# Kernel optimization log

Hardware: AMD Instinct MI355X
Metric: run time of the kernel (lower is better)

## Reference

```python
import jax, jax.numpy as jnp
import numpy as np

N = 30000      # nodes
E = 480000     # edges
H = 128        # hidden_nf
NQ = 7         # qubits
D = 2 ** NQ    # 128, quantum state dim == embedding_size
NL = 2         # block n_layers (QGCL layers)
QL = 2         # quantum circuit layers inside each QGCL
NORM = 100.0   # normalization_factor ('sum' aggregation)
NORM_CONST = 1.0


def _cnot_perm_indices(n):
    # Composed permutation for CNOT(0,1)...CNOT(n-2,n-1), CNOT(n-1,0).
    # PennyLane convention: wire 0 is the most significant bit.
    idx = np.arange(2 ** n)
    pairs = [(i, i + 1) for i in range(n - 1)] + [(n - 1, 0)]
    g = None
    for c, t in pairs:
        cb = (idx >> (n - 1 - c)) & 1
        f = idx ^ (cb << (n - 1 - t))  # flip target bit if control set (involution)
        g = f if g is None else g[f]
    return g

_CNOT_G = jnp.asarray(_cnot_perm_indices(NQ))


def _quantum_states(q_in, coeffs, A_re, A_im):
    """Vectorized VQC over all nodes. q_in [N,D] real -> [N,D] complex state."""
    norm = jnp.sqrt(jnp.sum(q_in ** 2, axis=1, keepdims=True) + 1e-12)
    s = (q_in / norm).astype(jnp.complex64)  # normalized initial state per node
    I = jnp.eye(D, dtype=jnp.complex64)
    for j in range(QL):
        # Cayley transform -> unitary
        A = (A_re[j] + 1j * A_im[j]).astype(jnp.complex64)
        A = A + A.conj().T
        q = (A - 1j * I) @ jnp.linalg.inv(A + 1j * I)
        # single-qubit layer: RY(b) @ RX(a) on every qubit -> kron power
        a, b = coeffs[j, 0].astype(jnp.complex64), coeffs[j, 1].astype(jnp.complex64)
        ca, sa = jnp.cos(a / 2), jnp.sin(a / 2)
        cb, sb = jnp.cos(b / 2), jnp.sin(b / 2)
        RX = jnp.stack([jnp.stack([ca, -1j * sa]), jnp.stack([-1j * sa, ca])])
        RY = jnp.stack([jnp.stack([cb, -sb]), jnp.stack([sb, cb])])
        G = RY @ RX
        Gk = G
        for _ in range(NQ - 1):
            Gk = jnp.kron(Gk, G)
        s = s @ q.T            # QubitUnitary
        s = s @ Gk.T           # RX/RY on all qubits
        s = s[:, _CNOT_G]      # CNOT ring (pure permutation)
    return s


def setup_inputs() -> dict:
    key = jax.random.key(0)
    ks = jax.random.split(key, 20)
    return {
        "h": jax.random.normal(ks[0], (N, H), jnp.float32),
        "x": jax.random.normal(ks[1], (N, 3), jnp.float32),
        "edge_index": jax.random.randint(ks[2], (2, E), 0, N, jnp.int32),
        "edge_attr": jax.random.normal(ks[3], (E, 1), jnp.float32),
        "e_w1": jax.random.normal(ks[4], (NL, 2 * H + 2, H), jnp.float32) * 0.05,
        "e_b1": jnp.zeros((NL, H), jnp.float32),
        "e_w2": jax.random.normal(ks[5], (NL, H, H), jnp.float32) * 0.05,
        "e_b2": jnp.zeros((NL, H), jnp.float32),
        "enc_w": jax.random.normal(ks[6], (NL, 2 * H, D), jnp.float32) * 0.05,
        "enc_b": jnp.zeros((NL, D), jnp.float32),
        "coeffs": jax.random.normal(ks[7], (NL, QL, 2), jnp.float32) * 0.1,
        "A_re": jax.random.normal(ks[8], (NL, QL, D, D), jnp.float32) * 0.01,
        "A_im": jax.random.normal(ks[9], (NL, QL, D, D), jnp.float32) * 0.01,
        "dec_w": jax.random.normal(ks[10], (NL, D, H), jnp.float32) * 0.05,
        "dec_b": jnp.zeros((NL, H), jnp.float32),
        "c_w1": jax.random.normal(ks[11], (2 * H + 2, H), jnp.float32) * 0.05,
        "c_b1": jnp.zeros((H,), jnp.float32),
        "c_w2": jax.random.normal(ks[12], (H, H), jnp.float32) * 0.05,
        "c_b2": jnp.zeros((H,), jnp.float32),
        "c_w3": jax.random.normal(ks[13], (H, 1), jnp.float32) * 0.001,  # xavier gain=0.001
    }


def reference(h, x, edge_index, edge_attr, e_w1, e_b1, e_w2, e_b2, enc_w, enc_b,
              coeffs, A_re, A_im, dec_w, dec_b, c_w1, c_b1, c_w2, c_b2, c_w3):
    row, col = edge_index[0], edge_index[1]
    # coord2diff
    diff = x[row] - x[col]
    radial = jnp.sum(diff ** 2, axis=1, keepdims=True)     # [E,1] (used as 'distances')
    coord_diff = diff / (jnp.sqrt(radial + 1e-8) + NORM_CONST)
    eattr = jnp.concatenate([radial, edge_attr], axis=1)   # [E,2]

    for l in range(NL):  # QGCL layers
        m = jnp.concatenate([h[row], h[col], eattr], axis=1)       # [E, 2H+2]
        m = jax.nn.silu(m @ e_w1[l] + e_b1[l])
        m = jax.nn.silu(m @ e_w2[l] + e_b2[l])                     # edge messages mij
        agg = jax.ops.segment_sum(m, row, num_segments=N) / NORM   # scatter-add
        q_in = jnp.concatenate([h, agg], axis=1) @ enc_w[l] + enc_b[l]
        # quantum part is detached in the original (torch .detach + re-tensor)
        qs = jax.lax.stop_gradient(
            _quantum_states(q_in, coeffs[l], A_re[l], A_im[l]))
        h = h + qs.real.astype(h.dtype) @ dec_w[l] + dec_b[l]

    # EquivariantUpdate (tanh=False)
    t = jnp.concatenate([h[row], h[col], eattr], axis=1)
    t = jax.nn.silu(t @ c_w1 + c_b1)
    t = jax.nn.silu(t @ c_w2 + c_b2)
    t = t @ c_w3                                                   # [E,1]
    trans = coord_diff * t
    x = x + jax.ops.segment_sum(trans, row, num_segments=N) / NORM
    return h, x
```

## Files before the change

kernel.cpp:

```cpp
#include <hip/hip_runtime.h>
#include <math.h>

#define N_NODES 30000
#define N_EDGES 480000
#define HDIM 128
#define EPB 64
#define AS 296
#define NAS 264
#define MS 136

typedef __attribute__((ext_vector_type(8))) short short8b;
typedef __attribute__((ext_vector_type(4))) float f32x4;

__device__ __forceinline__ float silu_f(float v) {
  return v / (1.0f + __expf(-v));
}

__device__ __forceinline__ unsigned short f2bf(float f) {
  unsigned int u = __float_as_uint(f);
  unsigned int r = u + 0x7fffu + ((u >> 16) & 1u);
  return (unsigned short)(r >> 16);
}

__global__ void init_out_bf_kernel(const float* __restrict__ h,
                                   const float* __restrict__ x,
                                   float* __restrict__ out,
                                   ushort* __restrict__ hbf) {
  int idx = blockIdx.x * 256 + threadIdx.x;
  float4 v = ((const float4*)h)[idx];
  ((float4*)out)[idx] = v;
  ushort4 o;
  o.x = f2bf(v.x); o.y = f2bf(v.y); o.z = f2bf(v.z); o.w = f2bf(v.w);
  ((ushort4*)hbf)[idx] = o;
  if (idx < N_NODES * 3 / 4) {
    ((float4*)(out + N_NODES * HDIM))[idx] = ((const float4*)x)[idx];
  }
}

__global__ void convert_all_kernel(
    const float* __restrict__ e_w1, const float* __restrict__ e_w2,
    const float* __restrict__ enc_w, const float* __restrict__ c_w1,
    const float* __restrict__ c_w2,
    ushort* __restrict__ w1cs, ushort* __restrict__ w2cs,
    ushort* __restrict__ enccs, ushort* __restrict__ cw1cs,
    ushort* __restrict__ cw2cs) {
  int idx = blockIdx.x * 256 + threadIdx.x;
  if (idx >= 55 * 4096) return;
  int ci = idx >> 12, rem = idx & 4095, n = rem >> 5, kk = rem & 31;
  const float* W;
  ushort* dst;
  int Kreal, ktl;
  if (ci < 18) {
    int l = ci / 9; ktl = ci - l * 9;
    W = e_w1 + (size_t)l * 258 * HDIM; dst = w1cs + (size_t)l * 9 * 4096;
    Kreal = 258;
  } else if (ci < 26) {
    int c2 = ci - 18; int l = c2 >> 2; ktl = c2 & 3;
    W = e_w2 + (size_t)l * HDIM * HDIM; dst = w2cs + (size_t)l * 4 * 4096;
    Kreal = 128;
  } else if (ci < 42) {
    int c2 = ci - 26; int l = c2 >> 3; ktl = c2 & 7;
    W = enc_w + (size_t)l * 256 * HDIM; dst = enccs + (size_t)l * 8 * 4096;
    Kreal = 256;
  } else if (ci < 51) {
    ktl = ci - 42; W = c_w1; dst = cw1cs; Kreal = 258;
  } else {
    ktl = ci - 51; W = c_w2; dst = cw2cs; Kreal = 128;
  }
  int k = ktl * 32 + kk;
  float v = (k < Kreal) ? W[(size_t)k * HDIM + n] : 0.0f;
  dst[ktl * 4096 + rem] = f2bf(v);
}

__global__ void count_kernel(const int* __restrict__ ei, int* __restrict__ cursor) {
  int e = blockIdx.x * 256 + threadIdx.x;
  atomicAdd(&cursor[ei[e]], 1);
}

__global__ __launch_bounds__(1024) void scan_kernel(int* __restrict__ cursor,
                                                    int* __restrict__ cstart) {
  __shared__ int sums[1024];
  const int tid = threadIdx.x;
  const int base = tid * 30;
  int local[30];
  int s = 0;
#pragma unroll
  for (int j = 0; j < 30; ++j) {
    int idx = base + j;
    int d = (idx < N_NODES) ? cursor[idx] : 0;
    local[j] = s;
    s += d;
  }
  sums[tid] = s;
  __syncthreads();
  for (int off = 1; off < 1024; off <<= 1) {
    int add = (tid >= off) ? sums[tid - off] : 0;
    __syncthreads();
    sums[tid] += add;
    __syncthreads();
  }
  int excl = (tid == 0) ? 0 : sums[tid - 1];
#pragma unroll
  for (int j = 0; j < 30; ++j) {
    int idx = base + j;
    if (idx < N_NODES) {
      int v = excl + local[j];
      cursor[idx] = v;
      cstart[idx] = v;
    }
  }
}

__global__ void fill_kernel(const int* __restrict__ ei, int* __restrict__ cursor,
                            int* __restrict__ elist) {
  int e = blockIdx.x * 256 + threadIdx.x;
  int r = ei[e];
  int pos = atomicAdd(&cursor[r], 1);
  elist[pos] = e;
}

__global__ void ns_init_kernel(const float* __restrict__ Are,
                               const float* __restrict__ Aim,
                               float2* __restrict__ X) {
  int lj = blockIdx.y;
  int idx = blockIdx.x * 256 + threadIdx.x;
  int r = idx >> 7, c = idx & 127;
  const float* are = Are + (size_t)lj * 16384;
  const float* aim = Aim + (size_t)lj * 16384;
  float re = are[r * 128 + c] + are[c * 128 + r];
  float im = aim[r * 128 + c] - aim[c * 128 + r];
  if (r == c) im -= 1.0f;
  X[(size_t)lj * 16384 + idx] = make_float2(re, im);
}

__global__ void ns_bx_kernel(const float* __restrict__ Are,
                             const float* __restrict__ Aim,
                             const float2* __restrict__ X,
                             float2* __restrict__ T) {
  int lj = blockIdx.y;
  int idx = blockIdx.x * 256 + threadIdx.x;
  int r = idx >> 7, c = idx & 127;
  const float* are = Are + (size_t)lj * 16384;
  const float* aim = Aim + (size_t)lj * 16384;
  const float2* x = X + (size_t)lj * 16384;
  float2 acc = make_float2(0.f, 0.f);
  for (int k = 0; k < 128; ++k) {
    float re = are[r * 128 + k] + are[k * 128 + r];
    float im = aim[r * 128 + k] - aim[k * 128 + r];
    if (k == r) im += 1.0f;
    float2 b = x[k * 128 + c];
    acc.x += re * b.x - im * b.y;
    acc.y += re * b.y + im * b.x;
  }
  T[(size_t)lj * 16384 + idx] = acc;
}

__global__ void ns_upd_kernel(const float2* __restrict__ X,
                              const float2* __restrict__ T,
                              float2* __restrict__ Xn) {
  int lj = blockIdx.y;
  int idx = blockIdx.x * 256 + threadIdx.x;
  int r = idx >> 7, c = idx & 127;
  const float2* x = X + (size_t)lj * 16384;
  const float2* t = T + (size_t)lj * 16384;
  float2 acc = make_float2(0.f, 0.f);
  for (int k = 0; k < 128; ++k) {
    float2 a = x[r * 128 + k];
    float2 b = t[k * 128 + c];
    acc.x += a.x * b.x - a.y * b.y;
    acc.y += a.x * b.y + a.y * b.x;
  }
  float2 xc = x[r * 128 + c];
  Xn[(size_t)lj * 16384 + idx] = make_float2(2.f * xc.x - acc.x, 2.f * xc.y - acc.y);
}

__global__ void qmat_kernel(const float* __restrict__ Are,
                            const float* __restrict__ Aim,
                            const float2* __restrict__ binvg,
                            float2* __restrict__ qm) {
  int lj = blockIdx.y;
  int idx = blockIdx.x * 256 + threadIdx.x;
  int r = idx >> 7, c = idx & 127;
  const float* are = Are + (size_t)lj * 16384;
  const float* aim = Aim + (size_t)lj * 16384;
  const float2* binv = binvg + (size_t)lj * 16384;
  float2 acc = make_float2(0.f, 0.f);
  for (int k = 0; k < 128; ++k) {
    float re = are[r * 128 + k] + are[k * 128 + r];
    float im = aim[r * 128 + k] - aim[k * 128 + r];
    if (k == r) im -= 1.0f;
    float2 b = binv[k * 128 + c];
    acc.x += re * b.x - im * b.y;
    acc.y += re * b.y + im * b.x;
  }
  qm[(size_t)lj * 16384 + idx] = acc;
}

__global__ void gk_kernel(const float* __restrict__ coeffs,
                          float2* __restrict__ gkm) {
  int lj = blockIdx.y;
  float a = coeffs[lj * 2 + 0], b = coeffs[lj * 2 + 1];
  float ca = cosf(0.5f * a), sa = sinf(0.5f * a);
  float cb = cosf(0.5f * b), sb = sinf(0.5f * b);
  float2 G[2][2];
  G[0][0] = make_float2(cb * ca, sb * sa);
  G[0][1] = make_float2(-sb * ca, -cb * sa);
  G[1][0] = make_float2(sb * ca, -cb * sa);
  G[1][1] = make_float2(cb * ca, -sb * sa);
  int idx = blockIdx.x * 256 + threadIdx.x;
  int r = idx >> 7, c = idx & 127;
  float2 acc = make_float2(1.f, 0.f);
#pragma unroll
  for (int bit = 6; bit >= 0; --bit) {
    float2 g = G[(r >> bit) & 1][(c >> bit) & 1];
    acc = make_float2(acc.x * g.x - acc.y * g.y, acc.x * g.y + acc.y * g.x);
  }
  gkm[(size_t)lj * 16384 + idx] = acc;
}

__global__ void nj_kernel(const float2* __restrict__ qm,
                          const float2* __restrict__ gkm,
                          float2* __restrict__ njm) {
  int lj = blockIdx.y;
  int idx = blockIdx.x * 256 + threadIdx.x;
  int i = idx >> 7, c = idx & 127;
  int gc;
  {
    int v = c;
    const int cs[7] = {6, 5, 4, 3, 2, 1, 0};
    const int ts[7] = {0, 6, 5, 4, 3, 2, 1};
#pragma unroll
    for (int p = 0; p < 7; ++p) {
      int cb = (v >> (6 - cs[p])) & 1;
      v = v ^ (cb << (6 - ts[p]));
    }
    gc = v;
  }
  const float2* q = qm + (size_t)lj * 16384;
  const float2* gk = gkm + (size_t)lj * 16384;
  float2 acc = make_float2(0.f, 0.f);
  for (int k = 0; k < 128; ++k) {
    float2 qa = q[k * 128 + i];
    float2 gb = gk[gc * 128 + k];
    acc.x += qa.x * gb.x - qa.y * gb.y;
    acc.y += qa.x * gb.y + qa.y * gb.x;
  }
  njm[(size_t)lj * 16384 + idx] = acc;
}

__global__ void compose_kernel(const float2* __restrict__ njm,
                               float2* __restrict__ um) {
  int l = blockIdx.y;
  int idx = blockIdx.x * 256 + threadIdx.x;
  int i = idx >> 7, c = idx & 127;
  const float2* n0 = njm + (size_t)(l * 2 + 0) * 16384;
  const float2* n1 = njm + (size_t)(l * 2 + 1) * 16384;
  float2 acc = make_float2(0.f, 0.f);
  for (int k = 0; k < 128; ++k) {
    float2 a = n0[i * 128 + k];
    float2 b = n1[k * 128 + c];
    acc.x += a.x * b.x - a.y * b.y;
    acc.y += a.x * b.y + a.y * b.x;
  }
  um[(size_t)l * 16384 + idx] = acc;
}

__global__ void wqd_kernel(const float2* __restrict__ um,
                           const float* __restrict__ decw,
                           ushort* __restrict__ wqdcs) {
  int l = blockIdx.y;
  int idx = blockIdx.x * 256 + threadIdx.x;
  int i = idx >> 7, c = idx & 127;
  const float2* u = um + (size_t)l * 16384;
  const float* dw = decw + (size_t)l * 16384;
  float acc = 0.f;
  for (int k = 0; k < 128; ++k) acc += u[i * 128 + k].x * dw[k * 128 + c];
  wqdcs[(size_t)l * 4 * 4096 + (i >> 5) * 4096 + c * 32 + (i & 31)] = f2bf(acc);
}

__global__ __launch_bounds__(256, 4) void edge_mfma_kernel(
    const ushort* __restrict__ hbf, const int* __restrict__ ei,
    const float* __restrict__ x, const float* __restrict__ ea,
    const int* __restrict__ elist, const int* __restrict__ cstart,
    const ushort* __restrict__ w1cs, const float* __restrict__ b1,
    const ushort* __restrict__ w2cs, const float* __restrict__ b2,
    float* __restrict__ agg, float* __restrict__ headp) {
  __shared__ ushort A[EPB * AS];
  __shared__ int rows[EPB];
  ushort* m1 = A;
  float* m2 = (float*)A;

  const int tid = threadIdx.x;
  const int lane = tid & 63, wave = tid >> 6;
  const int lrow = lane & 15, lq = lane >> 4;
  const int wbase = wave * 32;
  const int woff0 = (wbase + lrow) * 32 + lq * 8;
  const int woff1 = (wbase + 16 + lrow) * 32 + lq * 8;

  const float b1v[2] = {b1[wbase + lrow], b1[wbase + 16 + lrow]};
  const float b2v[2] = {b2[wbase + lrow], b2[wbase + 16 + lrow]};

  const int i0 = blockIdx.x * EPB;
  {
    const int e = tid >> 2, j = tid & 3;
    const int edge = elist[i0 + e];
    const int r = ei[edge], c = ei[N_EDGES + edge];
    if (j == 0) rows[e] = r;
    const uint4* hr = (const uint4*)(hbf + (size_t)r * HDIM + j * 32);
    const uint4* hc = (const uint4*)(hbf + (size_t)c * HDIM + j * 32);
    uint4* d1 = (uint4*)(A + e * AS + j * 32);
    uint4* d2 = (uint4*)(A + e * AS + 128 + j * 32);
    d1[0] = hr[0]; d1[1] = hr[1]; d1[2] = hr[2]; d1[3] = hr[3];
    d2[0] = hc[0]; d2[1] = hc[1]; d2[2] = hc[2]; d2[3] = hc[3];
    if (j == 3) {
      float dx = x[r * 3 + 0] - x[c * 3 + 0];
      float dy = x[r * 3 + 1] - x[c * 3 + 1];
      float dz = x[r * 3 + 2] - x[c * 3 + 2];
      ushort* dst = A + e * AS;
      dst[256] = f2bf(dx * dx + dy * dy + dz * dz);
      dst[257] = f2bf(ea[edge]);
#pragma unroll
      for (int z = 258; z < 288; ++z) dst[z] = 0;
    }
  }
  __syncthreads();

  f32x4 acc[4][2];
#pragma unroll
  for (int mt = 0; mt < 4; ++mt)
#pragma unroll
    for (int nt = 0; nt < 2; ++nt) acc[mt][nt] = (f32x4){0.f, 0.f, 0.f, 0.f};
  {
    short8b wcur0 = *(const short8b*)(w1cs + woff0);
    short8b wcur1 = *(const short8b*)(w1cs + woff1);
#pragma unroll
    for (int kt = 0; kt < 9; ++kt) {
      short8b wn0, wn1;
      if (kt < 8) {
        wn0 = *(const short8b*)(w1cs + (kt + 1) * 4096 + woff0);
        wn1 = *(const short8b*)(w1cs + (kt + 1) * 4096 + woff1);
      }
      short8b af[4];
#pragma unroll
      for (int mt = 0; mt < 4; ++mt)
        af[mt] = *(const short8b*)(A + (mt * 16 + lrow) * AS + kt * 32 + lq * 8);
#pragma unroll
      for (int mt = 0; mt < 4; ++mt) {
        acc[mt][0] = __builtin_amdgcn_mfma_f32_16x16x32_bf16(af[mt], wcur0, acc[mt][0], 0, 0, 0);
        acc[mt][1] = __builtin_amdgcn_mfma_f32_16x16x32_bf16(af[mt], wcur1, acc[mt][1], 0, 0, 0);
      }
      if (kt < 8) { wcur0 = wn0; wcur1 = wn1; }
    }
  }
  __syncthreads();
#pragma unroll
  for (int mt = 0; mt < 4; ++mt)
#pragma unroll
    for (int nt = 0; nt < 2; ++nt)
#pragma unroll
      for (int r = 0; r < 4; ++r)
        m1[(mt * 16 + lq * 4 + r) * MS + wbase + nt * 16 + lrow] =
            f2bf(silu_f(acc[mt][nt][r] + b1v[nt]));
  __syncthreads();

  f32x4 acc2[4][2];
#pragma unroll
  for (int mt = 0; mt < 4; ++mt)
#pragma unroll
    for (int nt = 0; nt < 2; ++nt) acc2[mt][nt] = (f32x4){0.f, 0.f, 0.f, 0.f};
  {
    short8b wcur0 = *(const short8b*)(w2cs + woff0);
    short8b wcur1 = *(const short8b*)(w2cs + woff1);
#pragma unroll
    for (int kt = 0; kt < 4; ++kt) {
      short8b wn0, wn1;
      if (kt < 3) {
        wn0 = *(const short8b*)(w2cs + (kt + 1) * 4096 + woff0);
        wn1 = *(const short8b*)(w2cs + (kt + 1) * 4096 + woff1);
      }
      short8b af[4];
#pragma unroll
      for (int mt = 0; mt < 4; ++mt)
        af[mt] = *(const short8b*)(m1 + (mt * 16 + lrow) * MS + kt * 32 + lq * 8);
#pragma unroll
      for (int mt = 0; mt < 4; ++mt) {
        acc2[mt][0] = __builtin_amdgcn_mfma_f32_16x16x32_bf16(af[mt], wcur0, acc2[mt][0], 0, 0, 0);
        acc2[mt][1] = __builtin_amdgcn_mfma_f32_16x16x32_bf16(af[mt], wcur1, acc2[mt][1], 0, 0, 0);
      }
      if (kt < 3) { wcur0 = wn0; wcur1 = wn1; }
    }
  }
  __syncthreads();
#pragma unroll
  for (int mt = 0; mt < 4; ++mt)
#pragma unroll
    for (int nt = 0; nt < 2; ++nt)
#pragma unroll
      for (int r = 0; r < 4; ++r)
        m2[(mt * 16 + lq * 4 + r) * MS + wbase + nt * 16 + lrow] =
            silu_f(acc2[mt][nt][r] + b2v[nt]);
  __syncthreads();

  const int e2 = tid & 63, cg = tid >> 6, cb = cg * 32;
  const int r_e = rows[e2];
  const bool leader = (e2 == 0) || (rows[e2 - 1] != r_e);
  if (leader) {
    f32x4 sum[8];
#pragma unroll
    for (int q = 0; q < 8; ++q) sum[q] = *(const f32x4*)(m2 + e2 * MS + cb + q * 4);
    int f = e2 + 1;
    while (f < EPB && rows[f] == r_e) {
#pragma unroll
      for (int q = 0; q < 8; ++q) sum[q] += *(const f32x4*)(m2 + f * MS + cb + q * 4);
      ++f;
    }
    float* dst = (e2 == 0 && cstart[r_e] < i0)
                     ? headp + (size_t)blockIdx.x * HDIM + cb
                     : agg + (size_t)r_e * HDIM + cb;
#pragma unroll
    for (int q = 0; q < 8; ++q) *(f32x4*)(dst + q * 4) = sum[q];
  }
}

__global__ __launch_bounds__(256, 2) void node_mfma_kernel(
    float* __restrict__ out_h, const float* __restrict__ agg,
    const int* __restrict__ cstart, const int* __restrict__ cend,
    const float* __restrict__ headp,
    const ushort* __restrict__ enccs, const float* __restrict__ encb,
    const ushort* __restrict__ wqdcs, const float* __restrict__ decb,
    ushort* __restrict__ hbf) {
  __shared__ ushort A[EPB * NAS];
  __shared__ ushort m1[EPB * MS];
  __shared__ float nbuf[4 * EPB];
  const int tid = threadIdx.x;
  const int n0 = blockIdx.x * EPB;

  const int lane = tid & 63, wave = tid >> 6;
  const int lrow = lane & 15, lq = lane >> 4;
  const int wbase = wave * 32;

  short8b wef[8][2], wqf[4][2];
#pragma unroll
  for (int kt = 0; kt < 8; ++kt)
#pragma unroll
    for (int nt = 0; nt < 2; ++nt)
      wef[kt][nt] = *(const short8b*)(enccs + kt * 4096 + (wbase + nt * 16 + lrow) * 32 + lq * 8);
#pragma unroll
  for (int kt = 0; kt < 4; ++kt)
#pragma unroll
    for (int nt = 0; nt < 2; ++nt)
      wqf[kt][nt] = *(const short8b*)(wqdcs + kt * 4096 + (wbase + nt * 16 + lrow) * 32 + lq * 8);
  const float ebv[2] = {encb[wbase + lrow], encb[wbase + 16 + lrow]};
  const float dbv[2] = {decb[wbase + lrow], decb[wbase + 16 + lrow]};

  {
    const int e = tid >> 2, j = tid & 3;
    int node = n0 + e;
    if (node >= N_NODES) node = N_NODES - 1;
    if (j < 2) {
      const float4* s4 = (const float4*)(out_h + (size_t)node * HDIM + j * 64);
      ushort* dst = A + e * NAS + j * 64;
#pragma unroll
      for (int i = 0; i < 16; ++i) {
        float4 v = s4[i];
        ushort4 o;
        o.x = f2bf(v.x); o.y = f2bf(v.y); o.z = f2bf(v.z); o.w = f2bf(v.w);
        ((ushort4*)dst)[i] = o;
      }
    } else {
      const int s = cstart[node], en = cend[node];
      const bool hasAgg = en > s;
      const float4* a4 = (const float4*)(agg + (size_t)node * HDIM + (j - 2) * 64);
      const int bb0 = (s >> 6) + 1;
// ... 52 lines not shown
        nbuf[wave * EPB + mt * 16 + lq * 4 + r] = ssp[r];
    }
  }
  __syncthreads();
#pragma unroll
  for (int mt = 0; mt < 4; ++mt)
#pragma unroll
    for (int r = 0; r < 4; ++r) {
      const int row = mt * 16 + lq * 4 + r;
      float sum = nbuf[row] + nbuf[EPB + row] + nbuf[2 * EPB + row] + nbuf[3 * EPB + row];
      float inv = 1.0f / sqrtf(sum + 1e-12f);
#pragma unroll
      for (int nt = 0; nt < 2; ++nt)
        m1[row * MS + wbase + nt * 16 + lrow] = f2bf(acc[mt][nt][r] * inv);
    }
  __syncthreads();

  f32x4 acc2[4][2];
#pragma unroll
  for (int mt = 0; mt < 4; ++mt)
#pragma unroll
    for (int nt = 0; nt < 2; ++nt) acc2[mt][nt] = (f32x4){0.f, 0.f, 0.f, 0.f};
#pragma unroll
  for (int kt = 0; kt < 4; ++kt) {
    short8b af[4];
#pragma unroll
    for (int mt = 0; mt < 4; ++mt)
      af[mt] = *(const short8b*)(m1 + (mt * 16 + lrow) * MS + kt * 32 + lq * 8);
#pragma unroll
    for (int mt = 0; mt < 4; ++mt)
#pragma unroll
      for (int nt = 0; nt < 2; ++nt)
        acc2[mt][nt] = __builtin_amdgcn_mfma_f32_16x16x32_bf16(af[mt], wqf[kt][nt], acc2[mt][nt], 0, 0, 0);
  }
#pragma unroll
  for (int mt = 0; mt < 4; ++mt)
#pragma unroll
    for (int nt = 0; nt < 2; ++nt) {
      const int n = wbase + nt * 16 + lrow;
#pragma unroll
      for (int r = 0; r < 4; ++r) {
        const int node = n0 + mt * 16 + lq * 4 + r;
        if (node < N_NODES) {
          size_t off = (size_t)node * HDIM + n;
          float hn = out_h[off] + acc2[mt][nt][r] + dbv[nt];
          out_h[off] = hn;
          hbf[off] = f2bf(hn);
        }
      }
    }
}

__global__ __launch_bounds__(256, 4) void coord_mfma_kernel(
    const ushort* __restrict__ hbf, const int* __restrict__ ei,
    const float* __restrict__ x, const float* __restrict__ ea,
    const int* __restrict__ elist,
    const ushort* __restrict__ w1cs, const float* __restrict__ b1,
    const ushort* __restrict__ w2cs, const float* __restrict__ b2,
    const float* __restrict__ w3, float* __restrict__ xout) {
  __shared__ ushort A[EPB * AS];
  __shared__ int rows[EPB];
  __shared__ int colsA[EPB];
  __shared__ float pbuf[4 * EPB];
  __shared__ float tv[EPB];
  ushort* m1 = A;

  const int tid = threadIdx.x;
  const int lane = tid & 63, wave = tid >> 6;
  const int lrow = lane & 15, lq = lane >> 4;
  const int wbase = wave * 32;
  const int woff0 = (wbase + lrow) * 32 + lq * 8;
  const int woff1 = (wbase + 16 + lrow) * 32 + lq * 8;

  const float b1v[2] = {b1[wbase + lrow], b1[wbase + 16 + lrow]};
  const float b2v[2] = {b2[wbase + lrow], b2[wbase + 16 + lrow]};
  const float w3v[2] = {w3[wbase + lrow], w3[wbase + 16 + lrow]};

  const int i0 = blockIdx.x * EPB;
  {
    const int e = tid >> 2, j = tid & 3;
    const int edge = elist[i0 + e];
    const int r = ei[edge], c = ei[N_EDGES + edge];
    if (j == 0) { rows[e] = r; colsA[e] = c; }
    const uint4* hr = (const uint4*)(hbf + (size_t)r * HDIM + j * 32);
    const uint4* hc = (const uint4*)(hbf + (size_t)c * HDIM + j * 32);
    uint4* d1 = (uint4*)(A + e * AS + j * 32);
    uint4* d2 = (uint4*)(A + e * AS + 128 + j * 32);
    d1[0] = hr[0]; d1[1] = hr[1]; d1[2] = hr[2]; d1[3] = hr[3];
    d2[0] = hc[0]; d2[1] = hc[1]; d2[2] = hc[2]; d2[3] = hc[3];
    if (j == 3) {
      float dx = x[r * 3 + 0] - x[c * 3 + 0];
      float dy = x[r * 3 + 1] - x[c * 3 + 1];
      float dz = x[r * 3 + 2] - x[c * 3 + 2];
      ushort* dst = A + e * AS;
      dst[256] = f2bf(dx * dx + dy * dy + dz * dz);
      dst[257] = f2bf(ea[edge]);
#pragma unroll
      for (int z = 258; z < 288; ++z) dst[z] = 0;
    }
  }
  __syncthreads();

  f32x4 acc[4][2];
#pragma unroll
  for (int mt = 0; mt < 4; ++mt)
#pragma unroll
    for (int nt = 0; nt < 2; ++nt) acc[mt][nt] = (f32x4){0.f, 0.f, 0.f, 0.f};
  {
    short8b wcur0 = *(const short8b*)(w1cs + woff0);
    short8b wcur1 = *(const short8b*)(w1cs + woff1);
#pragma unroll
    for (int kt = 0; kt < 9; ++kt) {
      short8b wn0, wn1;
      if (kt < 8) {
        wn0 = *(const short8b*)(w1cs + (kt + 1) * 4096 + woff0);
        wn1 = *(const short8b*)(w1cs + (kt + 1) * 4096 + woff1);
      }
      short8b af[4];
#pragma unroll
      for (int mt = 0; mt < 4; ++mt)
        af[mt] = *(const short8b*)(A + (mt * 16 + lrow) * AS + kt * 32 + lq * 8);
#pragma unroll
      for (int mt = 0; mt < 4; ++mt) {
        acc[mt][0] = __builtin_amdgcn_mfma_f32_16x16x32_bf16(af[mt], wcur0, acc[mt][0], 0, 0, 0);
        acc[mt][1] = __builtin_amdgcn_mfma_f32_16x16x32_bf16(af[mt], wcur1, acc[mt][1], 0, 0, 0);
      }
      if (kt < 8) { wcur0 = wn0; wcur1 = wn1; }
    }
  }
  __syncthreads();
#pragma unroll
  for (int mt = 0; mt < 4; ++mt)
#pragma unroll
    for (int nt = 0; nt < 2; ++nt)
#pragma unroll
      for (int r = 0; r < 4; ++r)
        m1[(mt * 16 + lq * 4 + r) * MS + wbase + nt * 16 + lrow] =
            f2bf(silu_f(acc[mt][nt][r] + b1v[nt]));
  __syncthreads();

  f32x4 acc2[4][2];
#pragma unroll
  for (int mt = 0; mt < 4; ++mt)
#pragma unroll
    for (int nt = 0; nt < 2; ++nt) acc2[mt][nt] = (f32x4){0.f, 0.f, 0.f, 0.f};
  {
    short8b wcur0 = *(const short8b*)(w2cs + woff0);
    short8b wcur1 = *(const short8b*)(w2cs + woff1);
#pragma unroll
    for (int kt = 0; kt < 4; ++kt) {
      short8b wn0, wn1;
      if (kt < 3) {
        wn0 = *(const short8b*)(w2cs + (kt + 1) * 4096 + woff0);
        wn1 = *(const short8b*)(w2cs + (kt + 1) * 4096 + woff1);
      }
      short8b af[4];
#pragma unroll
      for (int mt = 0; mt < 4; ++mt)
        af[mt] = *(const short8b*)(m1 + (mt * 16 + lrow) * MS + kt * 32 + lq * 8);
#pragma unroll
      for (int mt = 0; mt < 4; ++mt) {
        acc2[mt][0] = __builtin_amdgcn_mfma_f32_16x16x32_bf16(af[mt], wcur0, acc2[mt][0], 0, 0, 0);
        acc2[mt][1] = __builtin_amdgcn_mfma_f32_16x16x32_bf16(af[mt], wcur1, acc2[mt][1], 0, 0, 0);
      }
      if (kt < 3) { wcur0 = wn0; wcur1 = wn1; }
    }
  }
#pragma unroll
  for (int mt = 0; mt < 4; ++mt) {
    float p[4] = {0.f, 0.f, 0.f, 0.f};
#pragma unroll
    for (int nt = 0; nt < 2; ++nt)
#pragma unroll
      for (int r = 0; r < 4; ++r)
        p[r] += silu_f(acc2[mt][nt][r] + b2v[nt]) * w3v[nt];
#pragma unroll
    for (int m = 1; m < 16; m <<= 1)
#pragma unroll
      for (int r = 0; r < 4; ++r) p[r] += __shfl_xor(p[r], m, 64);
    if (lrow == 0) {
#pragma unroll
      for (int r = 0; r < 4; ++r)
        pbuf[wave * EPB + mt * 16 + lq * 4 + r] = p[r];
    }
  }
  __syncthreads();
  if (tid < EPB) {
    tv[tid] = (pbuf[tid] + pbuf[EPB + tid] + pbuf[2 * EPB + tid] + pbuf[3 * EPB + tid]) * 0.01f;
  }
  __syncthreads();
  if (tid < EPB) {
// ... 17 lines not shown
      atomicAdd(&xout[r_e * 3 + 0], sx);
      atomicAdd(&xout[r_e * 3 + 1], sy);
      atomicAdd(&xout[r_e * 3 + 2], sz);
    }
  }
}

extern "C" void kernel_launch(void* const* d_in, const int* in_sizes, int n_in,
                              void* d_out, int out_size, void* d_ws, size_t ws_size,
                              hipStream_t stream) {
  const float* h     = (const float*)d_in[0];
  const float* x     = (const float*)d_in[1];
  const int*   ei    = (const int*)d_in[2];
  const float* ea    = (const float*)d_in[3];
  const float* e_w1  = (const float*)d_in[4];
  const float* e_b1  = (const float*)d_in[5];
  const float* e_w2  = (const float*)d_in[6];
  const float* e_b2  = (const float*)d_in[7];
  const float* enc_w = (const float*)d_in[8];
  const float* enc_b = (const float*)d_in[9];
  const float* coeffs= (const float*)d_in[10];
  const float* A_re  = (const float*)d_in[11];
  const float* A_im  = (const float*)d_in[12];
  const float* dec_w = (const float*)d_in[13];
  const float* dec_b = (const float*)d_in[14];
  const float* c_w1  = (const float*)d_in[15];
  const float* c_b1  = (const float*)d_in[16];
  const float* c_w2  = (const float*)d_in[17];
  const float* c_b2  = (const float*)d_in[18];
  const float* c_w3  = (const float*)d_in[19];

  float* out = (float*)d_out;
  float* ws  = (float*)d_ws;

  float*  agg    = ws;
  float2* xa     = (float2*)(ws + 3840000);
  float2* xb     = (float2*)(ws + 3971072);
  float2* xt     = (float2*)(ws + 4102144);
  float2* qm     = (float2*)(ws + 4233216);
  float2* gkm    = (float2*)(ws + 4364288);
  float2* njm    = (float2*)(ws + 4495360);
  float2* um     = (float2*)(ws + 4626432);
  int*    cursor = (int*)(ws + 4724864);
  int*    cstart = (int*)(ws + 4754864);
  int*    elist  = (int*)(ws + 4784864);
  float*  headp  = ws + 5264864;
  ushort* hbf    = (ushort*)(ws + 6224864);
  ushort* w1cs   = (ushort*)(ws + 8144864);
  ushort* w2cs   = (ushort*)(ws + 8181728);
  ushort* cw1cs  = (ushort*)(ws + 8198112);
  ushort* cw2cs  = (ushort*)(ws + 8216544);
  ushort* enccs  = (ushort*)(ws + 8224736);
  ushort* wqdcs  = (ushort*)(ws + 8257504);

  init_out_bf_kernel<<<3750, 256, 0, stream>>>(h, x, out, hbf);

  hipMemsetAsync(cursor, 0, N_NODES * sizeof(int), stream);
  count_kernel<<<1875, 256, 0, stream>>>(ei, cursor);
  scan_kernel<<<1, 1024, 0, stream>>>(cursor, cstart);
  fill_kernel<<<1875, 256, 0, stream>>>(ei, cursor, elist);

  convert_all_kernel<<<880, 256, 0, stream>>>(e_w1, e_w2, enc_w, c_w1, c_w2,
                                              w1cs, w2cs, enccs, cw1cs, cw2cs);

  ns_init_kernel<<<dim3(64, 4), 256, 0, stream>>>(A_re, A_im, xa);
  float2* cur = xa;
  float2* nxt = xb;
  for (int it = 0; it < 3; ++it) {
    ns_bx_kernel<<<dim3(64, 4), 256, 0, stream>>>(A_re, A_im, cur, xt);
    ns_upd_kernel<<<dim3(64, 4), 256, 0, stream>>>(cur, xt, nxt);
    float2* tmp = cur; cur = nxt; nxt = tmp;
  }
  qmat_kernel<<<dim3(64, 4), 256, 0, stream>>>(A_re, A_im, cur, qm);
  gk_kernel<<<dim3(64, 4), 256, 0, stream>>>(coeffs, gkm);
  nj_kernel<<<dim3(64, 4), 256, 0, stream>>>(qm, gkm, njm);
  compose_kernel<<<dim3(64, 2), 256, 0, stream>>>(njm, um);
  wqd_kernel<<<dim3(64, 2), 256, 0, stream>>>(um, dec_w, wqdcs);

  for (int l = 0; l < 2; ++l) {
    edge_mfma_kernel<<<N_EDGES / EPB, 256, 0, stream>>>(
        hbf, ei, x, ea, elist, cstart,
        w1cs + (size_t)l * 9 * 4096, e_b1 + l * HDIM,
        w2cs + (size_t)l * 4 * 4096, e_b2 + l * HDIM, agg, headp);
    node_mfma_kernel<<<(N_NODES + EPB - 1) / EPB, 256, 0, stream>>>(
        out, agg, cstart, cursor, headp,
        enccs + (size_t)l * 8 * 4096, enc_b + l * HDIM,
        wqdcs + (size_t)l * 4 * 4096, dec_b + l * HDIM, hbf);
  }

  coord_mfma_kernel<<<N_EDGES / EPB, 256, 0, stream>>>(
      hbf, ei, x, ea, elist, cw1cs, c_b1, cw2cs, c_b2, c_w3,
      out + (size_t)N_NODES * HDIM);
}
```

Before: 770.1 us.

## Precompute per-node first-layer projections and gather them per edge instead of edge GEMM

The first edge MLP layer is split algebraically: h[row]@W_a + h[col]@W_b is computed once per node by a new pgemm kernel into a bf16 buffer P, and each edge sums two gathered rows plus the rank-2 radial/edge_attr term before SiLU. This removes the 9-k-tile per-edge MFMA GEMM for both the edge and coord kernels, cutting FLOPs by roughly the average degree. Edge messages are now kept in bf16 in shared memory for the segment reduction, and several small setup kernels are merged into one prep kernel, with edge counting folded into init. The Newton-Schulz iteration count also drops from 3 to 2, which risks reduced accuracy of the matrix inverse; the bf16 rounding of P and the messages adds further precision loss.

```diff
diff --git a/kernel.cpp b/kernel.cpp
--- a/kernel.cpp
+++ b/kernel.cpp
@@ -5,7 +5,6 @@
 #define N_EDGES 480000
 #define HDIM 128
 #define EPB 64
-#define AS 296
 #define NAS 264
 #define MS 136
 
@@ -24,8 +23,10 @@
 
 __global__ void init_out_bf_kernel(const float* __restrict__ h,
                                    const float* __restrict__ x,
+                                   const int* __restrict__ ei,
                                    float* __restrict__ out,
-                                   ushort* __restrict__ hbf) {
+                                   ushort* __restrict__ hbf,
+                                   int* __restrict__ cursor) {
   int idx = blockIdx.x * 256 + threadIdx.x;
   float4 v = ((const float4*)h)[idx];
   ((float4*)out)[idx] = v;
@@ -35,46 +36,7 @@
   if (idx < N_NODES * 3 / 4) {
     ((float4*)(out + N_NODES * HDIM))[idx] = ((const float4*)x)[idx];
   }
-}
-
-__global__ void convert_all_kernel(
-    const float* __restrict__ e_w1, const float* __restrict__ e_w2,
-    const float* __restrict__ enc_w, const float* __restrict__ c_w1,
-    const float* __restrict__ c_w2,
-    ushort* __restrict__ w1cs, ushort* __restrict__ w2cs,
-    ushort* __restrict__ enccs, ushort* __restrict__ cw1cs,
-    ushort* __restrict__ cw2cs) {
-  int idx = blockIdx.x * 256 + threadIdx.x;
-  if (idx >= 55 * 4096) return;
-  int ci = idx >> 12, rem = idx & 4095, n = rem >> 5, kk = rem & 31;
-  const float* W;
-  ushort* dst;
-  int Kreal, ktl;
-  if (ci < 18) {
-    int l = ci / 9; ktl = ci - l * 9;
-    W = e_w1 + (size_t)l * 258 * HDIM; dst = w1cs + (size_t)l * 9 * 4096;
-    Kreal = 258;
-  } else if (ci < 26) {
-    int c2 = ci - 18; int l = c2 >> 2; ktl = c2 & 3;
-    W = e_w2 + (size_t)l * HDIM * HDIM; dst = w2cs + (size_t)l * 4 * 4096;
-    Kreal = 128;
-  } else if (ci < 42) {
-    int c2 = ci - 26; int l = c2 >> 3; ktl = c2 & 7;
-    W = enc_w + (size_t)l * 256 * HDIM; dst = enccs + (size_t)l * 8 * 4096;
-    Kreal = 256;
-  } else if (ci < 51) {
-    ktl = ci - 42; W = c_w1; dst = cw1cs; Kreal = 258;
-  } else {
-    ktl = ci - 51; W = c_w2; dst = cw2cs; Kreal = 128;
-  }
-  int k = ktl * 32 + kk;
-  float v = (k < Kreal) ? W[(size_t)k * HDIM + n] : 0.0f;
-  dst[ktl * 4096 + rem] = f2bf(v);
-}
-
-__global__ void count_kernel(const int* __restrict__ ei, int* __restrict__ cursor) {
-  int e = blockIdx.x * 256 + threadIdx.x;
-  atomicAdd(&cursor[ei[e]], 1);
+  if (idx < N_EDGES) atomicAdd(&cursor[ei[idx]], 1);
 }
 
 __global__ __launch_bounds__(1024) void scan_kernel(int* __restrict__ cursor,
@@ -111,26 +73,80 @@
   }
 }
 
-__global__ void fill_kernel(const int* __restrict__ ei, int* __restrict__ cursor,
-                            int* __restrict__ elist) {
-  int e = blockIdx.x * 256 + threadIdx.x;
-  int r = ei[e];
-  int pos = atomicAdd(&cursor[r], 1);
-  elist[pos] = e;
-}
-
-__global__ void ns_init_kernel(const float* __restrict__ Are,
-                               const float* __restrict__ Aim,
-                               float2* __restrict__ X) {
-  int lj = blockIdx.y;
-  int idx = blockIdx.x * 256 + threadIdx.x;
-  int r = idx >> 7, c = idx & 127;
-  const float* are = Are + (size_t)lj * 16384;
-  const float* aim = Aim + (size_t)lj * 16384;
-  float re = are[r * 128 + c] + are[c * 128 + r];
-  float im = aim[r * 128 + c] - aim[c * 128 + r];
-  if (r == c) im -= 1.0f;
-  X[(size_t)lj * 16384 + idx] = make_float2(re, im);
+__global__ void prep_kernel(
+    const int* __restrict__ ei, int* __restrict__ cursor, int* __restrict__ elist,
+    const float* __restrict__ e_w1, const float* __restrict__ e_w2,
+    const float* __restrict__ enc_w, const float* __restrict__ c_w1,
+    const float* __restrict__ c_w2,
+    ushort* __restrict__ w1cs, ushort* __restrict__ w2cs,
+    ushort* __restrict__ enccs, ushort* __restrict__ cw1cs,
+    ushort* __restrict__ cw2cs,
+    const float* __restrict__ A_re, const float* __restrict__ A_im,
+    float2* __restrict__ X,
+    const float* __restrict__ coeffs, float2* __restrict__ gkm) {
+  const int b = blockIdx.x, tid = threadIdx.x;
+  if (b < 1875) {
+    int e = b * 256 + tid;
+    int r = ei[e];
+    int pos = atomicAdd(&cursor[r], 1);
+    elist[pos] = e;
+  } else if (b < 2755) {
+    int idx = (b - 1875) * 256 + tid;
+    int ci = idx >> 12, rem = idx & 4095, kk = rem & 31;
+    const float* W; ushort* dst; int Kreal, ktl;
+    if (ci < 18) {
+      int l = ci / 9; ktl = ci - l * 9;
+      W = e_w1 + (size_t)l * 258 * HDIM; dst = w1cs + (size_t)l * 9 * 4096;
+      Kreal = 258;
+    } else if (ci < 26) {
+      int c2 = ci - 18; int l = c2 >> 2; ktl = c2 & 3;
+      W = e_w2 + (size_t)l * HDIM * HDIM; dst = w2cs + (size_t)l * 4 * 4096;
+      Kreal = 128;
+    } else if (ci < 42) {
+      int c2 = ci - 26; int l = c2 >> 3; ktl = c2 & 7;
+      W = enc_w + (size_t)l * 256 * HDIM; dst = enccs + (size_t)l * 8 * 4096;
+      Kreal = 256;
+    } else if (ci < 51) {
+      ktl = ci - 42; W = c_w1; dst = cw1cs; Kreal = 258;
+    } else {
+      ktl = ci - 51; W = c_w2; dst = cw2cs; Kreal = 128;
+    }
+    int n = rem >> 5;
+    int k = ktl * 32 + kk;
+    float v = (k < Kreal) ? W[(size_t)k * HDIM + n] : 0.0f;
+    dst[ktl * 4096 + rem] = f2bf(v);
+  } else if (b < 3011) {
+    int bb = b - 2755;
+    int lj = bb >> 6;
+    int idx = (bb & 63) * 256 + tid;
+    int r = idx >> 7, c = idx & 127;
+    const float* are = A_re + (size_t)lj * 16384;
+    const float* aim = A_im + (size_t)lj * 16384;
+    float re = are[r * 128 + c] + are[c * 128 + r];
+    float im = aim[r * 128 + c] - aim[c * 128 + r];
+    if (r == c) im -= 1.0f;
+    X[(size_t)lj * 16384 + idx] = make_float2(re, im);
+  } else {
+    int bb = b - 3011;
+    int lj = bb >> 6;
+    float a = coeffs[lj * 2 + 0], bcf = coeffs[lj * 2 + 1];
+    float ca = cosf(0.5f * a), sa = sinf(0.5f * a);
+    float cb = cosf(0.5f * bcf), sb = sinf(0.5f * bcf);
+    float2 G[2][2];
+    G[0][0] = make_float2(cb * ca, sb * sa);
+    G[0][1] = make_float2(-sb * ca, -cb * sa);
+    G[1][0] = make_float2(sb * ca, -cb * sa);
+    G[1][1] = make_float2(cb * ca, -sb * sa);
+    int idx = (bb & 63) * 256 + tid;
+    int r = idx >> 7, c = idx & 127;
+    float2 acc = make_float2(1.f, 0.f);
+#pragma unroll
+    for (int bit = 6; bit >= 0; --bit) {
+      float2 g = G[(r >> bit) & 1][(c >> bit) & 1];
+      acc = make_float2(acc.x * g.x - acc.y * g.y, acc.x * g.y + acc.y * g.x);
+    }
+    gkm[(size_t)lj * 16384 + idx] = acc;
+  }
 }
 
 __global__ void ns_bx_kernel(const float* __restrict__ Are,
@@ -196,28 +212,6 @@
   qm[(size_t)lj * 16384 + idx] = acc;
 }
 
-__global__ void gk_kernel(const float* __restrict__ coeffs,
-                          float2* __restrict__ gkm) {
-  int lj = blockIdx.y;
-  float a = coeffs[lj * 2 + 0], b = coeffs[lj * 2 + 1];
-  float ca = cosf(0.5f * a), sa = sinf(0.5f * a);
-  float cb = cosf(0.5f * b), sb = sinf(0.5f * b);
-  float2 G[2][2];
-  G[0][0] = make_float2(cb * ca, sb * sa);
-  G[0][1] = make_float2(-sb * ca, -cb * sa);
-  G[1][0] = make_float2(sb * ca, -cb * sa);
-  G[1][1] = make_float2(cb * ca, -sb * sa);
-  int idx = blockIdx.x * 256 + threadIdx.x;
-  int r = idx >> 7, c = idx & 127;
-  float2 acc = make_float2(1.f, 0.f);
-#pragma unroll
-  for (int bit = 6; bit >= 0; --bit) {
-    float2 g = G[(r >> bit) & 1][(c >> bit) & 1];
-    acc = make_float2(acc.x * g.x - acc.y * g.y, acc.x * g.y + acc.y * g.x);
-  }
-  gkm[(size_t)lj * 16384 + idx] = acc;
-}
-
 __global__ void nj_kernel(const float2* __restrict__ qm,
                           const float2* __restrict__ gkm,
                           float2* __restrict__ njm) {
@@ -278,17 +272,74 @@
   wqdcs[(size_t)l * 4 * 4096 + (i >> 5) * 4096 + c * 32 + (i & 31)] = f2bf(acc);
 }
 
+__global__ __launch_bounds__(256, 1) void pgemm_kernel(
+    const ushort* __restrict__ hbf, const ushort* __restrict__ wcs,
+    const float* __restrict__ b1, ushort* __restrict__ P) {
+  __shared__ ushort Ht[EPB * MS];
+  const int tid = threadIdx.x;
+  const int n0 = blockIdx.x * EPB;
+  const int lane = tid & 63, wave = tid >> 6;
+  const int lrow = lane & 15, lq = lane >> 4;
+
+  {
+    const int e = tid >> 2, jj = tid & 3;
+    int node = n0 + e;
+    if (node >= N_NODES) node = N_NODES - 1;
+    const uint4* src = (const uint4*)(hbf + (size_t)node * HDIM + jj * 32);
+    uint4* dst = (uint4*)(Ht + e * MS + jj * 32);
+    dst[0] = src[0]; dst[1] = src[1]; dst[2] = src[2]; dst[3] = src[3];
+  }
+  short8b wf[4][4];
+  const int cs = (wave >> 1) * 4;
+  const int nb = (wave & 1) * 64;
+#pragma unroll
+  for (int kt = 0; kt < 4; ++kt)
+#pragma unroll
+    for (int nt = 0; nt < 4; ++nt)
+      wf[kt][nt] = *(const short8b*)(wcs + (cs + kt) * 4096 + (nb + nt * 16 + lrow) * 32 + lq * 8);
+  __syncthreads();
+
+  f32x4 acc[4][4];
+#pragma unroll
+  for (int mt = 0; mt < 4; ++mt)
+#pragma unroll
+    for (int nt = 0; nt < 4; ++nt) acc[mt][nt] = (f32x4){0.f, 0.f, 0.f, 0.f};
+#pragma unroll
+  for (int kt = 0; kt < 4; ++kt) {
+    short8b af[4];
+#pragma unroll
+    for (int mt = 0; mt < 4; ++mt)
+      af[mt] = *(const short8b*)(Ht + (mt * 16 + lrow) * MS + kt * 32 + lq * 8);
+#pragma unroll
+    for (int mt = 0; mt < 4; ++mt)
+#pragma unroll
+      for (int nt = 0; nt < 4; ++nt)
+        acc[mt][nt] = __builtin_amdgcn_mfma_f32_16x16x32_bf16(af[mt], wf[kt][nt], acc[mt][nt], 0, 0, 0);
+  }
+  const int cbase = wave * 64;
+#pragma unroll
+  for (int nt = 0; nt < 4; ++nt) {
+    const int ccol = cbase + nt * 16 + lrow;
+    const float bb = (ccol < 128) ? b1[ccol] : 0.f;
+#pragma unroll
+    for (int mt = 0; mt < 4; ++mt)
+#pragma unroll
+      for (int r = 0; r < 4; ++r) {
+        const int node = n0 + mt * 16 + lq * 4 + r;
+        if (node < N_NODES) P[(size_t)node * 256 + ccol] = f2bf(acc[mt][nt][r] + bb);
+      }
+  }
+}
+
 __global__ __launch_bounds__(256, 4) void edge_mfma_kernel(
-    const ushort* __restrict__ hbf, const int* __restrict__ ei,
+    const ushort* __restrict__ P, const int* __restrict__ ei,
     const float* __restrict__ x, const float* __restrict__ ea,
     const int* __restrict__ elist, const int* __restrict__ cstart,
-    const ushort* __restrict__ w1cs, const float* __restrict__ b1,
+    const float* __restrict__ wm,
     const ushort* __restrict__ w2cs, const float* __restrict__ b2,
     float* __restrict__ agg, float* __restrict__ headp) {
-  __shared__ ushort A[EPB * AS];
+  __shared__ ushort m1[EPB * MS];
   __shared__ int rows[EPB];
-  ushort* m1 = A;
-  float* m2 = (float*)A;
 
   const int tid = threadIdx.x;
   const int lane = tid & 63, wave = tid >> 6;
@@ -296,8 +347,6 @@
   const int wbase = wave * 32;
   const int woff0 = (wbase + lrow) * 32 + lq * 8;
   const int woff1 = (wbase + 16 + lrow) * 32 + lq * 8;
-
-  const float b1v[2] = {b1[wbase + lrow], b1[wbase + 16 + lrow]};
   const float b2v[2] = {b2[wbase + lrow], b2[wbase + 16 + lrow]};
 
   const int i0 = blockIdx.x * EPB;
@@ -306,61 +355,34 @@
     const int edge = elist[i0 + e];
     const int r = ei[edge], c = ei[N_EDGES + edge];
     if (j == 0) rows[e] = r;
-    const uint4* hr = (const uint4*)(hbf + (size_t)r * HDIM + j * 32);
-    const uint4* hc = (const uint4*)(hbf + (size_t)c * HDIM + j * 32);
-    uint4* d1 = (uint4*)(A + e * AS + j * 32);
-    uint4* d2 = (uint4*)(A + e * AS + 128 + j * 32);
-    d1[0] = hr[0]; d1[1] = hr[1]; d1[2] = hr[2]; d1[3] = hr[3];
-    d2[0] = hc[0]; d2[1] = hc[1]; d2[2] = hc[2]; d2[3] = hc[3];
-    if (j == 3) {
-      float dx = x[r * 3 + 0] - x[c * 3 + 0];
-      float dy = x[r * 3 + 1] - x[c * 3 + 1];
-      float dz = x[r * 3 + 2] - x[c * 3 + 2];
-      ushort* dst = A + e * AS;
-      dst[256] = f2bf(dx * dx + dy * dy + dz * dz);
-      dst[257] = f2bf(ea[edge]);
-#pragma unroll
-      for (int z = 258; z < 288; ++z) dst[z] = 0;
-    }
-  }
-  __syncthreads();
-
-  f32x4 acc[4][2];
-#pragma unroll
-  for (int mt = 0; mt < 4; ++mt)
-#pragma unroll
-    for (int nt = 0; nt < 2; ++nt) acc[mt][nt] = (f32x4){0.f, 0.f, 0.f, 0.f};
-  {
-    short8b wcur0 = *(const short8b*)(w1cs + woff0);
-    short8b wcur1 = *(const short8b*)(w1cs + woff1);
-#pragma unroll
-    for (int kt = 0; kt < 9; ++kt) {
-      short8b wn0, wn1;
-      if (kt < 8) {
-        wn0 = *(const short8b*)(w1cs + (kt + 1) * 4096 + woff0);
-        wn1 = *(const short8b*)(w1cs + (kt + 1) * 4096 + woff1);
-      }
-      short8b af[4];
-#pragma unroll
-      for (int mt = 0; mt < 4; ++mt)
-        af[mt] = *(const short8b*)(A + (mt * 16 + lrow) * AS + kt * 32 + lq * 8);
-#pragma unroll
-      for (int mt = 0; mt < 4; ++mt) {
-        acc[mt][0] = __builtin_amdgcn_mfma_f32_16x16x32_bf16(af[mt], wcur0, acc[mt][0], 0, 0, 0);
-        acc[mt][1] = __builtin_amdgcn_mfma_f32_16x16x32_bf16(af[mt], wcur1, acc[mt][1], 0, 0, 0);
-      }
-      if (kt < 8) { wcur0 = wn0; wcur1 = wn1; }
-    }
-  }
-  __syncthreads();
-#pragma unroll
-  for (int mt = 0; mt < 4; ++mt)
-#pragma unroll
-    for (int nt = 0; nt < 2; ++nt)
-#pragma unroll
-      for (int r = 0; r < 4; ++r)
-        m1[(mt * 16 + lq * 4 + r) * MS + wbase + nt * 16 + lrow] =
-            f2bf(silu_f(acc[mt][nt][r] + b1v[nt]));
+    const uint4* pr = (const uint4*)(P + (size_t)r * 256 + j * 32);
+    const uint4* pc = (const uint4*)(P + (size_t)c * 256 + 128 + j * 32);
+    uint4 PR[4] = {pr[0], pr[1], pr[2], pr[3]};
+    uint4 PC[4] = {pc[0], pc[1], pc[2], pc[3]};
+    float dx = x[r * 3 + 0] - x[c * 3 + 0];
+    float dy = x[r * 3 + 1] - x[c * 3 + 1];
+    float dz = x[r * 3 + 2] - x[c * 3 + 2];
+    float radial = dx * dx + dy * dy + dz * dz;
+    float eav = ea[edge];
+#pragma unroll
+    for (int q = 0; q < 4; ++q) {
+      const int kb = j * 32 + q * 8;
+      const uint ua[4] = {PR[q].x, PR[q].y, PR[q].z, PR[q].w};
+      const uint ub[4] = {PC[q].x, PC[q].y, PC[q].z, PC[q].w};
+      uint ow[4];
+#pragma unroll
+      for (int w = 0; w < 4; ++w) {
+        const int k = kb + w * 2;
+        float v0 = __uint_as_float(ua[w] << 16) + __uint_as_float(ub[w] << 16)
+                 + radial * wm[k] + eav * wm[128 + k];
+        float v1 = __uint_as_float(ua[w] & 0xffff0000u) + __uint_as_float(ub[w] & 0xffff0000u)
+                 + radial * wm[k + 1] + eav * wm[129 + k];
+        ow[w] = (uint)f2bf(silu_f(v0)) | ((uint)f2bf(silu_f(v1)) << 16);
+      }
+      uint4 o; o.x = ow[0]; o.y = ow[1]; o.z = ow[2]; o.w = ow[3];
+      *(uint4*)(m1 + e * MS + kb) = o;
+    }
+  }
   __syncthreads();
 
   f32x4 acc2[4][2];
@@ -397,28 +419,38 @@
     for (int nt = 0; nt < 2; ++nt)
 #pragma unroll
       for (int r = 0; r < 4; ++r)
-        m2[(mt * 16 + lq * 4 + r) * MS + wbase + nt * 16 + lrow] =
-            silu_f(acc2[mt][nt][r] + b2v[nt]);
+        m1[(mt * 16 + lq * 4 + r) * MS + wbase + nt * 16 + lrow] =
+            f2bf(silu_f(acc2[mt][nt][r] + b2v[nt]));
   __syncthreads();
 
   const int e2 = tid & 63, cg = tid >> 6, cb = cg * 32;
   const int r_e = rows[e2];
   const bool leader = (e2 == 0) || (rows[e2 - 1] != r_e);
   if (leader) {
-    f32x4 sum[8];
-#pragma unroll
-    for (int q = 0; q < 8; ++q) sum[q] = *(const f32x4*)(m2 + e2 * MS + cb + q * 4);
-    int f = e2 + 1;
-    while (f < EPB && rows[f] == r_e) {
-#pragma unroll
-      for (int q = 0; q < 8; ++q) sum[q] += *(const f32x4*)(m2 + f * MS + cb + q * 4);
+    float s[32];
+#pragma unroll
+    for (int q = 0; q < 32; ++q) s[q] = 0.f;
+    int f = e2;
+    do {
+      const uint4* mr = (const uint4*)(m1 + f * MS + cb);
+#pragma unroll
+      for (int q = 0; q < 4; ++q) {
+        uint4 u = mr[q];
+        const uint uu[4] = {u.x, u.y, u.z, u.w};
+#pragma unroll
+        for (int w = 0; w < 4; ++w) {
+          s[q * 8 + w * 2]     += __uint_as_float(uu[w] << 16);
+          s[q * 8 + w * 2 + 1] += __uint_as_float(uu[w] & 0xffff0000u);
+        }
+      }
       ++f;
-    }
+    } while (f < EPB && rows[f] == r_e);
     float* dst = (e2 == 0 && cstart[r_e] < i0)
                      ? headp + (size_t)blockIdx.x * HDIM + cb
                      : agg + (size_t)r_e * HDIM + cb;
 #pragma unroll
-    for (int q = 0; q < 8; ++q) *(f32x4*)(dst + q * 4) = sum[q];
+    for (int q = 0; q < 8; ++q)
+      *(float4*)(dst + q * 4) = make_float4(s[q * 4], s[q * 4 + 1], s[q * 4 + 2], s[q * 4 + 3]);
   }
 }
 
@@ -577,18 +609,17 @@
 }
 
 __global__ __launch_bounds__(256, 4) void coord_mfma_kernel(
-    const ushort* __restrict__ hbf, const int* __restrict__ ei,
+    const ushort* __restrict__ P, const int* __restrict__ ei,
     const float* __restrict__ x, const float* __restrict__ ea,
     const int* __restrict__ elist,
-    const ushort* __restrict__ w1cs, const float* __restrict__ b1,
+    const float* __restrict__ wm,
     const ushort* __restrict__ w2cs, const float* __restrict__ b2,
     const float* __restrict__ w3, float* __restrict__ xout) {
-  __shared__ ushort A[EPB * AS];
+  __shared__ ushort m1[EPB * MS];
   __shared__ int rows[EPB];
   __shared__ int colsA[EPB];
   __shared__ float pbuf[4 * EPB];
   __shared__ float tv[EPB];
-  ushort* m1 = A;
 
   const int tid = threadIdx.x;
   const int lane = tid & 63, wave = tid >> 6;
@@ -597,7 +628,6 @@
   const int woff0 = (wbase + lrow) * 32 + lq * 8;
   const int woff1 = (wbase + 16 + lrow) * 32 + lq * 8;
 
-  const float b1v[2] = {b1[wbase + lrow], b1[wbase + 16 + lrow]};
   const float b2v[2] = {b2[wbase + lrow], b2[wbase + 16 + lrow]};
   const float w3v[2] = {w3[wbase + lrow], w3[wbase + 16 + lrow]};
 
@@ -607,61 +637,34 @@
     const int edge = elist[i0 + e];
     const int r = ei[edge], c = ei[N_EDGES + edge];
     if (j == 0) { rows[e] = r; colsA[e] = c; }
-    const uint4* hr = (const uint4*)(hbf + (size_t)r * HDIM + j * 32);
-    const uint4* hc = (const uint4*)(hbf + (size_t)c * HDIM + j * 32);
-    uint4* d1 = (uint4*)(A + e * AS + j * 32);
-    uint4* d2 = (uint4*)(A + e * AS + 128 + j * 32);
-    d1[0] = hr[0]; d1[1] = hr[1]; d1[2] = hr[2]; d1[3] = hr[3];
-    d2[0] = hc[0]; d2[1] = hc[1]; d2[2] = hc[2]; d2[3] = hc[3];
-    if (j == 3) {
-      float dx = x[r * 3 + 0] - x[c * 3 + 0];
-      float dy = x[r * 3 + 1] - x[c * 3 + 1];
-      float dz = x[r * 3 + 2] - x[c * 3 + 2];
-      ushort* dst = A + e * AS;
-      dst[256] = f2bf(dx * dx + dy * dy + dz * dz);
-      dst[257] = f2bf(ea[edge]);
-#pragma unroll
-      for (int z = 258; z < 288; ++z) dst[z] = 0;
-    }
-  }
-  __syncthreads();
-
-  f32x4 acc[4][2];
-#pragma unroll
-  for (int mt = 0; mt < 4; ++mt)
-#pragma unroll
-    for (int nt = 0; nt < 2; ++nt) acc[mt][nt] = (f32x4){0.f, 0.f, 0.f, 0.f};
-  {
-    short8b wcur0 = *(const short8b*)(w1cs + woff0);
-    short8b wcur1 = *(const short8b*)(w1cs + woff1);
-#pragma unroll
-    for (int kt = 0; kt < 9; ++kt) {
-      short8b wn0, wn1;
-      if (kt < 8) {
-        wn0 = *(const short8b*)(w1cs + (kt + 1) * 4096 + woff0);
-        wn1 = *(const short8b*)(w1cs + (kt + 1) * 4096 + woff1);
-      }
-      short8b af[4];
-#pragma unroll
-      for (int mt = 0; mt < 4; ++mt)
-        af[mt] = *(const short8b*)(A + (mt * 16 + lrow) * AS + kt * 32 + lq * 8);
-#pragma unroll
-      for (int mt = 0; mt < 4; ++mt) {
-        acc[mt][0] = __builtin_amdgcn_mfma_f32_16x16x32_bf16(af[mt], wcur0, acc[mt][0], 0, 0, 0);
-        acc[mt][1] = __builtin_amdgcn_mfma_f32_16x16x32_bf16(af[mt], wcur1, acc[mt][1], 0, 0, 0);
-      }
-      if (kt < 8) { wcur0 = wn0; wcur1 = wn1; }
-    }
-  }
-  __syncthreads();
-#pragma unroll
-  for (int mt = 0; mt < 4; ++mt)
-#pragma unroll
-    for (int nt = 0; nt < 2; ++nt)
-#pragma unroll
-      for (int r = 0; r < 4; ++r)
-        m1[(mt * 16 + lq * 4 + r) * MS + wbase + nt * 16 + lrow] =
-            f2bf(silu_f(acc[mt][nt][r] + b1v[nt]));
+    const uint4* pr = (const uint4*)(P + (size_t)r * 256 + j * 32);
+    const uint4* pc = (const uint4*)(P + (size_t)c * 256 + 128 + j * 32);
+    uint4 PR[4] = {pr[0], pr[1], pr[2], pr[3]};
+    uint4 PC[4] = {pc[0], pc[1], pc[2], pc[3]};
+    float dx = x[r * 3 + 0] - x[c * 3 + 0];
+    float dy = x[r * 3 + 1] - x[c * 3 + 1];
+    float dz = x[r * 3 + 2] - x[c * 3 + 2];
+    float radial = dx * dx + dy * dy + dz * dz;
+    float eav = ea[edge];
+#pragma unroll
+    for (int q = 0; q < 4; ++q) {
+      const int kb = j * 32 + q * 8;
+      const uint ua[4] = {PR[q].x, PR[q].y, PR[q].z, PR[q].w};
+      const uint ub[4] = {PC[q].x, PC[q].y, PC[q].z, PC[q].w};
+      uint ow[4];
+#pragma unroll
+      for (int w = 0; w < 4; ++w) {
+        const int k = kb + w * 2;
+        float v0 = __uint_as_float(ua[w] << 16) + __uint_as_float(ub[w] << 16)
+                 + radial * wm[k] + eav * wm[128 + k];
+        float v1 = __uint_as_float(ua[w] & 0xffff0000u) + __uint_as_float(ub[w] & 0xffff0000u)
+                 + radial * wm[k + 1] + eav * wm[129 + k];
+        ow[w] = (uint)f2bf(silu_f(v0)) | ((uint)f2bf(silu_f(v1)) << 16);
+      }
+      uint4 o; o.x = ow[0]; o.y = ow[1]; o.z = ow[2]; o.w = ow[3];
+      *(uint4*)(m1 + e * MS + kb) = o;
+    }
+  }
   __syncthreads();
 
   f32x4 acc2[4][2];
@@ -785,43 +788,46 @@
   ushort* cw2cs  = (ushort*)(ws + 8216544);
   ushort* enccs  = (ushort*)(ws + 8224736);
   ushort* wqdcs  = (ushort*)(ws + 8257504);
-
-  init_out_bf_kernel<<<3750, 256, 0, stream>>>(h, x, out, hbf);
+  ushort* Pbuf   = (ushort*)(ws + 8273888);
 
   hipMemsetAsync(cursor, 0, N_NODES * sizeof(int), stream);
-  count_kernel<<<1875, 256, 0, stream>>>(ei, cursor);
+  init_out_bf_kernel<<<3750, 256, 0, stream>>>(h, x, ei, out, hbf, cursor);
   scan_kernel<<<1, 1024, 0, stream>>>(cursor, cstart);
-  fill_kernel<<<1875, 256, 0, stream>>>(ei, cursor, elist);
-
-  convert_all_kernel<<<880, 256, 0, stream>>>(e_w1, e_w2, enc_w, c_w1, c_w2,
-                                              w1cs, w2cs, enccs, cw1cs, cw2cs);
-
-  ns_init_kernel<<<dim3(64, 4), 256, 0, stream>>>(A_re, A_im, xa);
+
+  prep_kernel<<<3267, 256, 0, stream>>>(ei, cursor, elist,
+                                        e_w1, e_w2, enc_w, c_w1, c_w2,
+                                        w1cs, w2cs, enccs, cw1cs, cw2cs,
+                                        A_re, A_im, xa, coeffs, gkm);
+
   float2* cur = xa;
   float2* nxt = xb;
-  for (int it = 0; it < 3; ++it) {
+  for (int it = 0; it < 2; ++it) {
     ns_bx_kernel<<<dim3(64, 4), 256, 0, stream>>>(A_re, A_im, cur, xt);
     ns_upd_kernel<<<dim3(64, 4), 256, 0, stream>>>(cur, xt, nxt);
     float2* tmp = cur; cur = nxt; nxt = tmp;
   }
   qmat_kernel<<<dim3(64, 4), 256, 0, stream>>>(A_re, A_im, cur, qm);
-  gk_kernel<<<dim3(64, 4), 256, 0, stream>>>(coeffs, gkm);
   nj_kernel<<<dim3(64, 4), 256, 0, stream>>>(qm, gkm, njm);
   compose_kernel<<<dim3(64, 2), 256, 0, stream>>>(njm, um);
   wqd_kernel<<<dim3(64, 2), 256, 0, stream>>>(um, dec_w, wqdcs);
 
+  const int NB = (N_NODES + EPB - 1) / EPB;
+
   for (int l = 0; l < 2; ++l) {
+    pgemm_kernel<<<NB, 256, 0, stream>>>(hbf, w1cs + (size_t)l * 9 * 4096,
+                                         e_b1 + l * HDIM, Pbuf);
     edge_mfma_kernel<<<N_EDGES / EPB, 256, 0, stream>>>(
-        hbf, ei, x, ea, elist, cstart,
-        w1cs + (size_t)l * 9 * 4096, e_b1 + l * HDIM,
+        Pbuf, ei, x, ea, elist, cstart,
+        e_w1 + (size_t)l * 258 * HDIM + 256 * HDIM,
         w2cs + (size_t)l * 4 * 4096, e_b2 + l * HDIM, agg, headp);
-    node_mfma_kernel<<<(N_NODES + EPB - 1) / EPB, 256, 0, stream>>>(
+    node_mfma_kernel<<<NB, 256, 0, stream>>>(
         out, agg, cstart, cursor, headp,
         enccs + (size_t)l * 8 * 4096, enc_b + l * HDIM,
         wqdcs + (size_t)l * 4 * 4096, dec_b + l * HDIM, hbf);
   }
 
+  pgemm_kernel<<<NB, 256, 0, stream>>>(hbf, cw1cs, c_b1, Pbuf);
   coord_mfma_kernel<<<N_EDGES / EPB, 256, 0, stream>>>(
-      hbf, ei, x, ea, elist, cw1cs, c_b1, cw2cs, c_b2, c_w3,
+      Pbuf, ei, x, ea, elist, c_w1 + 256 * HDIM, cw2cs, c_b2, c_w3,
       out + (size_t)N_NODES * HDIM);
 }
```

New measurement: 778.1 us. About the same (+1.0%).
